# Optimization experiments

Measured on AMD Instinct MI355X. Metric: run time of the kernel, lower is better.

Reference implementation:

```python
import jax, jax.numpy as jnp
import numpy as np

N_EXPERTS = 64
TOP_K = 2
LOAD_BALANCE_COEF = 0.01
D_MODEL = 4096
N_TOKENS = 16384


def setup_inputs() -> dict:
    key = jax.random.key(0)
    kx, kw = jax.random.split(key)
    x = jax.random.normal(kx, (N_TOKENS, D_MODEL), dtype=jnp.float32)
    # nn.init.normal_(gate.weight, std=0.01); shape (n_experts, d_model)
    gate_w = 0.01 * jax.random.normal(kw, (N_EXPERTS, D_MODEL), dtype=jnp.float32)
    return {"x": x, "gate_w": gate_w}


def reference(x, gate_w):
    # logits: (N, n_experts)
    logits = jnp.einsum('nd,ed->ne', x, gate_w)
    router_probs = jax.nn.softmax(logits, axis=-1)
    top_k_weights, top_k_indices = jax.lax.top_k(router_probs, TOP_K)
    routing_weights = top_k_weights / jnp.sum(top_k_weights, axis=-1, keepdims=True)
    top1 = top_k_indices[:, 0]
    one_hot = jax.nn.one_hot(top1, N_EXPERTS, dtype=x.dtype)  # (N, n_experts)
    f_i = jnp.mean(one_hot, axis=0)          # fraction of tokens per expert (detached)
    p_i = jnp.mean(router_probs, axis=0)     # mean router prob per expert (diff.)
    load_balance_loss = LOAD_BALANCE_COEF * jnp.sum(jax.lax.stop_gradient(f_i) * p_i)
    return routing_weights, top_k_indices, load_balance_loss
```

## Files before the change

### kernel.cpp

```cpp
#include <hip/hip_runtime.h>
#include <hip/hip_bf16.h>
#include <math.h>

#define N_TOKENS 16384
#define D_MODEL  4096
#define N_EXP    64

#define BK     16
#define XS_LD  260
#define WS_LD  68
#define PB_BLOCKS 512

__global__ void __launch_bounds__(256)
router_gemm3(const float* __restrict__ x, const float* __restrict__ w,
             float* __restrict__ partial, int kslice) {
    __shared__ float xs[BK * XS_LD];
    __shared__ float ws[BK * WS_LD];

    int tid  = threadIdx.x;
    int tok0 = blockIdx.x * 256;
    int k0   = blockIdx.y * kslice;

    int wave = tid >> 6;
    int lane = tid & 63;
    int trow = wave * 64 + (lane & 7) * 8;
    int ecol = (lane >> 3) * 8;

    int s_sub = tid >> 2;
    int s_kc  = (tid & 3) * 4;

    float acc[8][8];
#pragma unroll
    for (int t = 0; t < 8; ++t)
#pragma unroll
        for (int e = 0; e < 8; ++e) acc[t][e] = 0.f;

    for (int kk = 0; kk < kslice; kk += BK) {
        const float* xsrc = x + (size_t)tok0 * D_MODEL + k0 + kk;
        const float* wsrc = w + k0 + kk;
        float4 xv0 = *(const float4*)(xsrc + (size_t)(s_sub +   0) * D_MODEL + s_kc);
        float4 xv1 = *(const float4*)(xsrc + (size_t)(s_sub +  64) * D_MODEL + s_kc);
        float4 xv2 = *(const float4*)(xsrc + (size_t)(s_sub + 128) * D_MODEL + s_kc);
        float4 xv3 = *(const float4*)(xsrc + (size_t)(s_sub + 192) * D_MODEL + s_kc);
        float4 wv  = *(const float4*)(wsrc + (size_t)s_sub * D_MODEL + s_kc);

        __syncthreads();

        xs[(s_kc + 0) * XS_LD + s_sub +   0] = xv0.x;
        xs[(s_kc + 1) * XS_LD + s_sub +   0] = xv0.y;
        xs[(s_kc + 2) * XS_LD + s_sub +   0] = xv0.z;
        xs[(s_kc + 3) * XS_LD + s_sub +   0] = xv0.w;
        xs[(s_kc + 0) * XS_LD + s_sub +  64] = xv1.x;
        xs[(s_kc + 1) * XS_LD + s_sub +  64] = xv1.y;
        xs[(s_kc + 2) * XS_LD + s_sub +  64] = xv1.z;
        xs[(s_kc + 3) * XS_LD + s_sub +  64] = xv1.w;
        xs[(s_kc + 0) * XS_LD + s_sub + 128] = xv2.x;
        xs[(s_kc + 1) * XS_LD + s_sub + 128] = xv2.y;
        xs[(s_kc + 2) * XS_LD + s_sub + 128] = xv2.z;
        xs[(s_kc + 3) * XS_LD + s_sub + 128] = xv2.w;
        xs[(s_kc + 0) * XS_LD + s_sub + 192] = xv3.x;
        xs[(s_kc + 1) * XS_LD + s_sub + 192] = xv3.y;
        xs[(s_kc + 2) * XS_LD + s_sub + 192] = xv3.z;
        xs[(s_kc + 3) * XS_LD + s_sub + 192] = xv3.w;
        ws[(s_kc + 0) * WS_LD + s_sub] = wv.x;
        ws[(s_kc + 1) * WS_LD + s_sub] = wv.y;
        ws[(s_kc + 2) * WS_LD + s_sub] = wv.z;
        ws[(s_kc + 3) * WS_LD + s_sub] = wv.w;

        __syncthreads();

#pragma unroll 4
        for (int k = 0; k < BK; ++k) {
            const float* xr = &xs[k * XS_LD + trow];
            const float* wr = &ws[k * WS_LD + ecol];
            float4 xa = *(const float4*)(xr);
            float4 xb = *(const float4*)(xr + 4);
            float4 wa = *(const float4*)(wr);
            float4 wb = *(const float4*)(wr + 4);
            float xf[8] = {xa.x, xa.y, xa.z, xa.w, xb.x, xb.y, xb.z, xb.w};
            float wf[8] = {wa.x, wa.y, wa.z, wa.w, wb.x, wb.y, wb.z, wb.w};
#pragma unroll
            for (int t = 0; t < 8; ++t)
#pragma unroll
                for (int e = 0; e < 8; ++e)
                    acc[t][e] = fmaf(xf[t], wf[e], acc[t][e]);
        }
    }

    float* po = partial + (size_t)blockIdx.y * (N_TOKENS * N_EXP)
                        + (size_t)(tok0 + trow) * N_EXP + ecol;
#pragma unroll
    for (int t = 0; t < 8; ++t) {
        *(float4*)(po + (size_t)t * N_EXP)     =
            make_float4(acc[t][0], acc[t][1], acc[t][2], acc[t][3]);
        *(float4*)(po + (size_t)t * N_EXP + 4) =
            make_float4(acc[t][4], acc[t][5], acc[t][6], acc[t][7]);
    }
}

__global__ void __launch_bounds__(256)
router_phaseB(const float* __restrict__ partial, int n_slices,
              float* __restrict__ out, float* __restrict__ block_sums) {
    __shared__ float p_acc[4][N_EXP];
    __shared__ float f_acc[4][N_EXP];

    int tid  = threadIdx.x;
    int wave = tid >> 6;
    int lane = tid & 63;

    p_acc[wave][lane] = 0.f;
    f_acc[wave][lane] = 0.f;

    for (int it = 0; it < 8; ++it) {
        int token = blockIdx.x * 32 + it * 4 + wave;

        float logit = 0.f;
        size_t base = (size_t)token * N_EXP + lane;
        for (int s = 0; s < n_slices; ++s)
            logit += partial[(size_t)s * (N_TOKENS * N_EXP) + base];

        float m = logit; int i1 = lane;
#pragma unroll
        for (int off = 1; off < 64; off <<= 1) {
            float ov = __shfl_xor(m, off, 64);
            int   oi = __shfl_xor(i1, off, 64);
            if (ov > m || (ov == m && oi < i1)) { m = ov; i1 = oi; }
        }

        float p = expf(logit - m);
        float denom = p;
#pragma unroll
        for (int off = 1; off < 64; off <<= 1)
            denom += __shfl_xor(denom, off, 64);

        p_acc[wave][lane] += p / denom;

        float l2 = (lane == i1) ? -__builtin_inff() : logit;
        int i2 = lane;
#pragma unroll
        for (int off = 1; off < 64; off <<= 1) {
            float ov = __shfl_xor(l2, off, 64);
            int   oi = __shfl_xor(i2, off, 64);
            if (ov > l2 || (ov == l2 && oi < i2)) { l2 = ov; i2 = oi; }
        }

        if (lane == i1) f_acc[wave][lane] += 1.f;

        if (lane == 0) {
            float p1 = 1.0f / denom;
            float p2 = expf(l2 - m) / denom;
            float s12 = p1 + p2;
            ((float2*)out)[token] = make_float2(p1 / s12, p2 / s12);
            ((float2*)(out + 2 * N_TOKENS))[token] =
                make_float2((float)i1, (float)i2);
        }
    }

    __syncthreads();
    if (tid < N_EXP) {
        float ps = p_acc[0][tid] + p_acc[1][tid] + p_acc[2][tid] + p_acc[3][tid];
        float fs = f_acc[0][tid] + f_acc[1][tid] + f_acc[2][tid] + f_acc[3][tid];
        block_sums[(size_t)blockIdx.x * 128 + tid]      = ps;
        block_sums[(size_t)blockIdx.x * 128 + 64 + tid] = fs;
    }
}

__global__ void __launch_bounds__(256)
router_final(const float* __restrict__ block_sums, float* __restrict__ out) {
    __shared__ float sp[4][N_EXP];
    __shared__ float sf[4][N_EXP];

    int tid  = threadIdx.x;
    int wave = tid >> 6;
    int lane = tid & 63;

    float ps = 0.f, fs = 0.f;
    for (int b = wave * (PB_BLOCKS / 4); b < (wave + 1) * (PB_BLOCKS / 4); ++b) {
        ps += block_sums[(size_t)b * 128 + lane];
        fs += block_sums[(size_t)b * 128 + 64 + lane];
    }
    sp[wave][lane] = ps;
    sf[wave][lane] = fs;
    __syncthreads();

    if (tid < N_EXP) {
        float pt = sp[0][tid] + sp[1][tid] + sp[2][tid] + sp[3][tid];
        float ft = sf[0][tid] + sf[1][tid] + sf[2][tid] + sf[3][tid];
        float v = pt * ft;
#pragma unroll
        for (int off = 1; off < 64; off <<= 1)
            v += __shfl_xor(v, off, 64);
        if (tid == 0)
            out[4 * N_TOKENS] = 0.01f * v / ((float)N_TOKENS * (float)N_TOKENS);
    }
}

extern "C" void kernel_launch(void* const* d_in, const int* in_sizes, int n_in,
                              void* d_out, int out_size, void* d_ws, size_t ws_size,
                              hipStream_t stream) {
    const float* x = (const float*)d_in[0];
    const float* w = (const float*)d_in[1];
    float* out = (float*)d_out;
    char* ws = (char*)d_ws;

    const size_t BS_BYTES = (size_t)PB_BLOCKS * 128 * sizeof(float);

    int ksplit = 1;
    for (int c = 16; c >= 1; c >>= 1) {
        size_t need = (size_t)c * N_TOKENS * N_EXP * sizeof(float) + BS_BYTES + 512;
        if (need <= ws_size) { ksplit = c; break; }
    }

    size_t partial_bytes = (size_t)ksplit * N_TOKENS * N_EXP * sizeof(float);
    float* partial = (float*)ws;
    float* block_sums = (float*)(ws + partial_bytes);

    dim3 gridA(N_TOKENS / 256, ksplit);
    router_gemm3<<<gridA, 256, 0, stream>>>(x, w, partial, D_MODEL / ksplit);

    router_phaseB<<<PB_BLOCKS, 256, 0, stream>>>(partial, ksplit, out, block_sums);

    router_final<<<1, 256, 0, stream>>>(block_sums, out);
}
```

Baseline: 449.4 us.

## Pre-transpose gate weights and read them as wave-uniform scalar loads in GEMM

Adds a small kernel that transposes the gate weights to a (d_model, experts) layout in workspace. The GEMM then drops the shared-memory weight tile and reads 16 weights per wave through wave-uniform (scalar) loads, with each thread computing 4 tokens by 16 experts. The goal is to cut LDS traffic and bank pressure for the weights and to free shared memory. In exchange it adds an extra kernel launch, uses more workspace (which may lower the k-split), and makes the x-from-LDS reuse per FMA less favourable than the previous 8x8 tile.

```diff
diff --git a/kernel.cpp b/kernel.cpp
--- a/kernel.cpp
+++ b/kernel.cpp
@@ -8,41 +8,44 @@
 
 #define BK     16
 #define XS_LD  260
-#define WS_LD  68
 #define PB_BLOCKS 512
 
+__global__ void router_transpose(const float* __restrict__ w,
+                                 float* __restrict__ wt) {
+    int idx = blockIdx.x * 256 + threadIdx.x;
+    int e = idx >> 12;
+    int d = idx & 4095;
+    wt[d * N_EXP + e] = w[idx];
+}
+
 __global__ void __launch_bounds__(256)
-router_gemm3(const float* __restrict__ x, const float* __restrict__ w,
+router_gemm4(const float* __restrict__ x, const float* __restrict__ wt,
              float* __restrict__ partial, int kslice) {
     __shared__ float xs[BK * XS_LD];
-    __shared__ float ws[BK * WS_LD];
 
     int tid  = threadIdx.x;
     int tok0 = blockIdx.x * 256;
     int k0   = blockIdx.y * kslice;
 
-    int wave = tid >> 6;
     int lane = tid & 63;
-    int trow = wave * 64 + (lane & 7) * 8;
-    int ecol = (lane >> 3) * 8;
+    int e0   = __builtin_amdgcn_readfirstlane((tid >> 6) * 16);
+    int t0   = lane * 4;
 
     int s_sub = tid >> 2;
     int s_kc  = (tid & 3) * 4;
 
-    float acc[8][8];
-#pragma unroll
-    for (int t = 0; t < 8; ++t)
-#pragma unroll
-        for (int e = 0; e < 8; ++e) acc[t][e] = 0.f;
+    float acc[4][16];
+#pragma unroll
+    for (int t = 0; t < 4; ++t)
+#pragma unroll
+        for (int j = 0; j < 16; ++j) acc[t][j] = 0.f;
 
     for (int kk = 0; kk < kslice; kk += BK) {
         const float* xsrc = x + (size_t)tok0 * D_MODEL + k0 + kk;
-        const float* wsrc = w + k0 + kk;
         float4 xv0 = *(const float4*)(xsrc + (size_t)(s_sub +   0) * D_MODEL + s_kc);
         float4 xv1 = *(const float4*)(xsrc + (size_t)(s_sub +  64) * D_MODEL + s_kc);
         float4 xv2 = *(const float4*)(xsrc + (size_t)(s_sub + 128) * D_MODEL + s_kc);
         float4 xv3 = *(const float4*)(xsrc + (size_t)(s_sub + 192) * D_MODEL + s_kc);
-        float4 wv  = *(const float4*)(wsrc + (size_t)s_sub * D_MODEL + s_kc);
 
         __syncthreads();
 
@@ -62,40 +65,34 @@
         xs[(s_kc + 1) * XS_LD + s_sub + 192] = xv3.y;
         xs[(s_kc + 2) * XS_LD + s_sub + 192] = xv3.z;
         xs[(s_kc + 3) * XS_LD + s_sub + 192] = xv3.w;
-        ws[(s_kc + 0) * WS_LD + s_sub] = wv.x;
-        ws[(s_kc + 1) * WS_LD + s_sub] = wv.y;
-        ws[(s_kc + 2) * WS_LD + s_sub] = wv.z;
-        ws[(s_kc + 3) * WS_LD + s_sub] = wv.w;
 
         __syncthreads();
 
-#pragma unroll 4
+        const float* wrow = wt + (size_t)(k0 + kk) * N_EXP + e0;
+
+#pragma unroll
         for (int k = 0; k < BK; ++k) {
-            const float* xr = &xs[k * XS_LD + trow];
-            const float* wr = &ws[k * WS_LD + ecol];
-            float4 xa = *(const float4*)(xr);
-            float4 xb = *(const float4*)(xr + 4);
-            float4 wa = *(const float4*)(wr);
-            float4 wb = *(const float4*)(wr + 4);
-            float xf[8] = {xa.x, xa.y, xa.z, xa.w, xb.x, xb.y, xb.z, xb.w};
-            float wf[8] = {wa.x, wa.y, wa.z, wa.w, wb.x, wb.y, wb.z, wb.w};
-#pragma unroll
-            for (int t = 0; t < 8; ++t)
-#pragma unroll
-                for (int e = 0; e < 8; ++e)
-                    acc[t][e] = fmaf(xf[t], wf[e], acc[t][e]);
+            float4 xa = *(const float4*)&xs[k * XS_LD + t0];
+            const float* wr = wrow + k * N_EXP;
+#pragma unroll
+            for (int j = 0; j < 16; ++j) {
+                float wv = wr[j];
+                acc[0][j] = fmaf(xa.x, wv, acc[0][j]);
+                acc[1][j] = fmaf(xa.y, wv, acc[1][j]);
+                acc[2][j] = fmaf(xa.z, wv, acc[2][j]);
+                acc[3][j] = fmaf(xa.w, wv, acc[3][j]);
+            }
         }
     }
 
     float* po = partial + (size_t)blockIdx.y * (N_TOKENS * N_EXP)
-                        + (size_t)(tok0 + trow) * N_EXP + ecol;
-#pragma unroll
-    for (int t = 0; t < 8; ++t) {
-        *(float4*)(po + (size_t)t * N_EXP)     =
-            make_float4(acc[t][0], acc[t][1], acc[t][2], acc[t][3]);
-        *(float4*)(po + (size_t)t * N_EXP + 4) =
-            make_float4(acc[t][4], acc[t][5], acc[t][6], acc[t][7]);
-    }
+                        + (size_t)(tok0 + t0) * N_EXP + e0;
+#pragma unroll
+    for (int t = 0; t < 4; ++t)
+#pragma unroll
+        for (int j = 0; j < 16; j += 4)
+            *(float4*)(po + (size_t)t * N_EXP + j) =
+                make_float4(acc[t][j], acc[t][j+1], acc[t][j+2], acc[t][j+3]);
 }
 
 __global__ void __launch_bounds__(256)
@@ -203,20 +200,25 @@
     float* out = (float*)d_out;
     char* ws = (char*)d_ws;
 
+    const size_t WT_BYTES = (size_t)D_MODEL * N_EXP * sizeof(float);
     const size_t BS_BYTES = (size_t)PB_BLOCKS * 128 * sizeof(float);
 
     int ksplit = 1;
     for (int c = 16; c >= 1; c >>= 1) {
-        size_t need = (size_t)c * N_TOKENS * N_EXP * sizeof(float) + BS_BYTES + 512;
+        size_t need = (size_t)c * N_TOKENS * N_EXP * sizeof(float)
+                      + WT_BYTES + BS_BYTES + 512;
         if (need <= ws_size) { ksplit = c; break; }
     }
 
     size_t partial_bytes = (size_t)ksplit * N_TOKENS * N_EXP * sizeof(float);
     float* partial = (float*)ws;
-    float* block_sums = (float*)(ws + partial_bytes);
+    float* wt = (float*)(ws + partial_bytes);
+    float* block_sums = (float*)(ws + partial_bytes + WT_BYTES);
+
+    router_transpose<<<(N_EXP * D_MODEL) / 256, 256, 0, stream>>>(w, wt);
 
     dim3 gridA(N_TOKENS / 256, ksplit);
-    router_gemm3<<<gridA, 256, 0, stream>>>(x, w, partial, D_MODEL / ksplit);
+    router_gemm4<<<gridA, 256, 0, stream>>>(x, wt, partial, D_MODEL / ksplit);
 
     router_phaseB<<<PB_BLOCKS, 256, 0, stream>>>(partial, ksplit, out, block_sums);
 
```

After: 469.9 us. 1.05x slower.
